# Performance work log

Measured on AMD Instinct MI355X. Metric: run time of the kernel, lower is better.

Reference implementation:

```python
import jax, jax.numpy as jnp
import numpy as np

EPS = 1e-6
MAX_TANH_ARG = 15.0


def setup_inputs() -> dict:
    key = jax.random.key(0)
    k1, k2, k3 = jax.random.split(key, 3)
    B, H, N, D = 2, 16, 2048, 64
    return {
        "q": jax.random.normal(k1, (B, H, N, D), dtype=jnp.float32),
        "k": jax.random.normal(k2, (B, H, N, D), dtype=jnp.float32),
        "v": jax.random.normal(k3, (B, H, N, D), dtype=jnp.float32),
        "c": jnp.ones((1,), dtype=jnp.float32),
        "beta": jnp.ones((1,), dtype=jnp.float32),
    }


def _exp_map(x, sqrt_c):
    # tangent space -> Poincare ball
    norm = jnp.maximum(jnp.linalg.norm(x, axis=-1, keepdims=True), EPS)
    tanh_arg = jnp.minimum(sqrt_c * norm, MAX_TANH_ARG)
    return x * (jnp.tanh(tanh_arg) / (sqrt_c * norm))


def reference(q, k, v, c, beta):
    # q, k, v: [B, H, N, D]; c, beta: [1] positive scalars
    causal, use_exp_map = True, True
    N = q.shape[2]
    c = jnp.maximum(c.astype(jnp.float32), EPS)  # [1]
    sqrt_c = jnp.sqrt(c)
    beta = beta.astype(jnp.float32)

    if use_exp_map:
        q_hyp = _exp_map(q, sqrt_c)
        k_hyp = _exp_map(k, sqrt_c)
    else:
        q_hyp, k_hyp = q, k

    q_n2 = jnp.sum(q_hyp * q_hyp, axis=-1, keepdims=True)          # [B,H,N,1]
    k_n2 = jnp.sum(k_hyp * k_hyp, axis=-1, keepdims=True)          # [B,H,N,1]
    qk = jnp.einsum('bhnd,bhmd->bhnm', q_hyp, k_hyp)               # [B,H,N,N]

    diff_n2 = jnp.maximum(q_n2 - 2.0 * qk + jnp.swapaxes(k_n2, -2, -1), 0.0)
    denom = jnp.maximum((1.0 - c * q_n2) * (1.0 - c * jnp.swapaxes(k_n2, -2, -1)), EPS)
    arg = jnp.maximum(1.0 + 2.0 * c * diff_n2 / denom, 1.0 + EPS)
    dist = jnp.arccosh(arg) / sqrt_c                               # Poincare distance
    scores = -beta * dist                                          # [B,H,N,N]

    if causal:
        mask = jnp.triu(jnp.ones((N, N), dtype=bool), k=1)
        scores = jnp.where(mask, -jnp.inf, scores)

    attn = jax.nn.softmax(scores, axis=-1)
    out = jnp.einsum('bhnm,bhmd->bhnd', attn, v)
    return out.astype(q.dtype)
```

## Files before the change

### kernel.cpp

```cpp
#include <hip/hip_runtime.h>
#include <hip/hip_bf16.h>

typedef __bf16 bf16x8 __attribute__((ext_vector_type(8)));
typedef float  f32x4  __attribute__((ext_vector_type(4)));

#define BDIM  2
#define HDIM  16
#define NDIM  2048
#define DDIM  64
#define BH    (BDIM*HDIM)
#define EPSF  1e-6f

#define QK_BLOCKS (BH * NDIM / 16)
#define V_BLOCKS  (BH * NDIM / 64)

__device__ __forceinline__ unsigned short f2bf(float x){
    union { float f; unsigned u; } a; a.f = x;
    unsigned r = a.u + 0x7fffu + ((a.u >> 16) & 1u);
    return (unsigned short)(r >> 16);
}

__global__ __launch_bounds__(256)
void prep(const float* __restrict__ q, const float* __restrict__ k,
          const float* __restrict__ v,
          unsigned short* __restrict__ qh, unsigned short* __restrict__ kh,
          unsigned short* __restrict__ vt,
          float* __restrict__ qn2, float* __restrict__ kn2,
          const float* __restrict__ cp)
{
    __shared__ float t[64][65];
    const int tid = threadIdx.x;

    if (blockIdx.x < QK_BLOCKS){
        const int row = blockIdx.x * 16 + (tid >> 4);
        const int c0  = (tid & 15) * 4;
        const float c   = fmaxf(cp[0], EPSF);
        const float sqc = sqrtf(c);

        {
            float4 x = *(const float4*)(q + (size_t)row * DDIM + c0);
            float ss = fmaf(x.x, x.x, fmaf(x.y, x.y, fmaf(x.z, x.z, x.w * x.w)));
            #pragma unroll
            for (int off = 1; off < 16; off <<= 1) ss += __shfl_xor(ss, off);
            float sn    = fmaxf(sqrtf(ss), EPSF);
            float targ  = fminf(sqc * sn, 15.0f);
            float e     = exp2f(targ * 2.885390082f);
            float th    = (e - 1.0f) * __builtin_amdgcn_rcpf(e + 1.0f);
            float scale = th * __builtin_amdgcn_rcpf(sqc * sn);
            ushort4 o;
            o.x = f2bf(x.x * scale); o.y = f2bf(x.y * scale);
            o.z = f2bf(x.z * scale); o.w = f2bf(x.w * scale);
            *(ushort4*)(qh + (size_t)row * DDIM + c0) = o;
            if ((tid & 15) == 0) qn2[row] = ss * scale * scale;
        }
        {
            float4 x = *(const float4*)(k + (size_t)row * DDIM + c0);
            float ss = fmaf(x.x, x.x, fmaf(x.y, x.y, fmaf(x.z, x.z, x.w * x.w)));
            #pragma unroll
            for (int off = 1; off < 16; off <<= 1) ss += __shfl_xor(ss, off);
            float sn    = fmaxf(sqrtf(ss), EPSF);
            float targ  = fminf(sqc * sn, 15.0f);
            float e     = exp2f(targ * 2.885390082f);
            float th    = (e - 1.0f) * __builtin_amdgcn_rcpf(e + 1.0f);
            float scale = th * __builtin_amdgcn_rcpf(sqc * sn);
            ushort4 o;
            o.x = f2bf(x.x * scale); o.y = f2bf(x.y * scale);
            o.z = f2bf(x.z * scale); o.w = f2bf(x.w * scale);
            *(ushort4*)(kh + (size_t)row * DDIM + c0) = o;
            if ((tid & 15) == 0) kn2[row] = ss * scale * scale;
        }
    } else {
        const int b  = blockIdx.x - QK_BLOCKS;
        const int bh = b >> 5;
        const int n0 = (b & 31) * 64;

        #pragma unroll
        for (int i = 0; i < 4; ++i){
            int ch  = tid + i * 256;
            int row = ch >> 4;
            int c4  = ch & 15;
            const float4 g = *(const float4*)(v + ((size_t)bh * NDIM + n0 + row) * DDIM + c4 * 4);
            t[row][c4*4 + 0] = g.x; t[row][c4*4 + 1] = g.y;
            t[row][c4*4 + 2] = g.z; t[row][c4*4 + 3] = g.w;
        }
        __syncthreads();
        #pragma unroll
        for (int i = 0; i < 4; ++i){
            int ch = tid + i * 256;
            int d  = ch >> 4;
            int nc = ch & 15;
            ushort4 o;
            o.x = f2bf(t[nc*4 + 0][d]); o.y = f2bf(t[nc*4 + 1][d]);
            o.z = f2bf(t[nc*4 + 2][d]); o.w = f2bf(t[nc*4 + 3][d]);
            *(ushort4*)(vt + ((size_t)bh * DDIM + d) * NDIM + n0 + nc * 4) = o;
        }
    }
}

__global__ __launch_bounds__(64, 4)
void hyp_attn(const unsigned short* __restrict__ qh, const unsigned short* __restrict__ kh,
              const unsigned short* __restrict__ vtg,
              const float* __restrict__ qn2g, const float* __restrict__ kn2g,
              const float* __restrict__ cp, const float* __restrict__ bp,
              float* __restrict__ out)
{
    __shared__ unsigned short pw[16 * 72];

    const int bh  = blockIdx.x;
    const int j   = 127 - (int)blockIdx.y;
    const int l   = threadIdx.x & 63;
    const int l15 = l & 15;
    const int lg  = l >> 4;

    const float c   = fmaxf(cp[0], EPSF);
    const float sqc = sqrtf(c);
    const float nb2 = -bp[0] / sqc;
    const float tc  = 2.0f * c;

    const unsigned short* khb  = kh  + (size_t)bh * (NDIM * DDIM);
    const unsigned short* vtb  = vtg + (size_t)bh * (NDIM * DDIM);
    const float*          kn2b = kn2g + (size_t)bh * NDIM;

    const int q0 = j * 16;
    const size_t qbase = ((size_t)bh * NDIM + (q0 + l15)) * DDIM;
    const bf16x8 qa0 = *(const bf16x8*)(qh + qbase + lg * 8);
    const bf16x8 qa1 = *(const bf16x8*)(qh + qbase + 32 + lg * 8);

    const int qr0 = q0 + lg * 4;
    float qn2r[4], omq[4];
    #pragma unroll
    for (int r = 0; r < 4; ++r){
        qn2r[r] = qn2g[(size_t)bh * NDIM + qr0 + r];
        omq[r]  = 1.0f - c * qn2r[r];
    }

    float m2[4], lr[4];
    f32x4 O[4];
    #pragma unroll
    for (int r = 0; r < 4; ++r){ m2[r] = -1e30f; lr[r] = 0.0f; }
    #pragma unroll
    for (int vd = 0; vd < 4; ++vd) O[vd] = (f32x4){0.f, 0.f, 0.f, 0.f};

    const int ktend = j >> 2;

    for (int kt = 0; kt <= ktend; ++kt){
        const int k0 = kt * 64;

        bf16x8 kf0[4], kf1[4];
        float  kn2m[4];
        #pragma unroll
        for (int f = 0; f < 4; ++f){
            const unsigned short* kp = khb + (size_t)(k0 + f * 16 + l15) * DDIM + lg * 8;
            kf0[f]  = *(const bf16x8*)(kp);
            kf1[f]  = *(const bf16x8*)(kp + 32);
            kn2m[f] = kn2b[k0 + f * 16 + l15];
        }

        f32x4 S[4];
        #pragma unroll
        for (int f = 0; f < 4; ++f){
            f32x4 acc = (f32x4){0.f, 0.f, 0.f, 0.f};
            acc = __builtin_amdgcn_mfma_f32_16x16x32_bf16(qa0, kf0[f], acc, 0, 0, 0);
            acc = __builtin_amdgcn_mfma_f32_16x16x32_bf16(qa1, kf1[f], acc, 0, 0, 0);
            S[f] = acc;
        }

        bf16x8 vf[2][4];
        #pragma unroll
        for (int mc = 0; mc < 2; ++mc)
            #pragma unroll
            for (int vd = 0; vd < 4; ++vd)
                vf[mc][vd] = *(const bf16x8*)(vtb + (size_t)(vd * 16 + l15) * NDIM
                                              + k0 + mc * 32 + lg * 8);

        #pragma unroll
        for (int f = 0; f < 4; ++f){
            const float kn2v = kn2m[f];
            const float omk  = 1.0f - c * kn2v;
            #pragma unroll
            for (int r = 0; r < 4; ++r){
                float diff = fmaf(-2.0f, S[f][r], qn2r[r] + kn2v);
                float den  = fmaxf(omq[r] * omk, EPSF);
                float arg  = fmaxf(fmaf(tc * diff, __builtin_amdgcn_rcpf(den), 1.0f), 1.0f + EPSF);
                float w    = arg + sqrtf(fmaf(arg, arg, -1.0f));
                S[f][r]    = nb2 * __log2f(w);
            }
        }
        if (kt == ktend){
            #pragma unroll
            for (int f = 0; f < 4; ++f){
                const int m = k0 + f * 16 + l15;
                #pragma unroll
                for (int r = 0; r < 4; ++r)
                    if (m > qr0 + r) S[f][r] = -1e30f;
            }
        }

        float rmax[4];
        #pragma unroll
        for (int r = 0; r < 4; ++r){
            rmax[r] = fmaxf(fmaxf(S[0][r], S[1][r]), fmaxf(S[2][r], S[3][r]));
            #pragma unroll
            for (int off = 1; off < 16; off <<= 1)
                rmax[r] = fmaxf(rmax[r], __shfl_xor(rmax[r], off));
        }
        bool up = (rmax[0] > m2[0]) | (rmax[1] > m2[1]) |
                  (rmax[2] > m2[2]) | (rmax[3] > m2[3]);
        if (__any(up)){
            #pragma unroll
            for (int r = 0; r < 4; ++r){
                float nm  = fmaxf(m2[r], rmax[r]);
                float scl = exp2f(m2[r] - nm);
                lr[r] *= scl; m2[r] = nm;
                #pragma unroll
                for (int vd = 0; vd < 4; ++vd) O[vd][r] *= scl;
            }
        }

        float psum[4] = {0.f, 0.f, 0.f, 0.f};
        #pragma unroll
        for (int f = 0; f < 4; ++f){
            const int fx = ((f ^ lg) << 4) + l15;
            #pragma unroll
            for (int r = 0; r < 4; ++r){
                float p = exp2f(S[f][r] - m2[r]);
                psum[r] += p;
                pw[(lg * 4 + r) * 72 + fx] = f2bf(p);
            }
        }
        #pragma unroll
        for (int r = 0; r < 4; ++r){
            #pragma unroll
            for (int off = 1; off < 16; off <<= 1)
                psum[r] += __shfl_xor(psum[r], off);
            lr[r] += psum[r];
        }

        asm volatile("s_waitcnt lgkmcnt(0)" ::: "memory");

        #pragma unroll
        for (int mc = 0; mc < 2; ++mc){
            const int f  = 2 * mc + (lg >> 1);
            const int fx = f ^ ((l15 >> 2) & 3);
            bf16x8 pa = *(const bf16x8*)&pw[l15 * 72 + fx * 16 + (lg & 1) * 8];
            #pragma unroll
            for (int vd = 0; vd < 4; ++vd)
                O[vd] = __builtin_amdgcn_mfma_f32_16x16x32_bf16(pa, vf[mc][vd], O[vd], 0, 0, 0);
        }
    }

    #pragma unroll
    for (int r = 0; r < 4; ++r){
        float rl = __builtin_amdgcn_rcpf(lr[r]);
        #pragma unroll
        for (int vd = 0; vd < 4; ++vd)
            out[((size_t)bh * NDIM + qr0 + r) * DDIM + vd * 16 + l15] = O[vd][r] * rl;
    }
}

extern "C" void kernel_launch(void* const* d_in, const int* in_sizes, int n_in,
                              void* d_out, int out_size, void* d_ws, size_t ws_size,
                              hipStream_t stream)
{
    const float* q   = (const float*)d_in[0];
    const float* k   = (const float*)d_in[1];
    const float* v   = (const float*)d_in[2];
    const float* cp  = (const float*)d_in[3];
    const float* bp  = (const float*)d_in[4];
    float*       out = (float*)d_out;

    char* ws = (char*)d_ws;
    const size_t elems = (size_t)BH * NDIM * DDIM;
    unsigned short* qh  = (unsigned short*)ws;  ws += elems * 2;
    unsigned short* kh  = (unsigned short*)ws;  ws += elems * 2;
    unsigned short* vt  = (unsigned short*)ws;  ws += elems * 2;
    float*          qn2 = (float*)ws;           ws += (size_t)BH * NDIM * 4;
    float*          kn2 = (float*)ws;

    prep<<<QK_BLOCKS + V_BLOCKS, 256, 0, stream>>>(q, k, v, qh, kh, vt, qn2, kn2, cp);
    hyp_attn<<<dim3(BH, 128), 64, 0, stream>>>(qh, kh, vt, qn2, kn2, cp, bp, out);
}
```

Measured before the change: 236.8 us.

## Compute softmax row sums via MFMA and pack two waves per block

Row sums of the softmax probabilities are now accumulated with an extra MFMA against a vector of bf16 ones. This replaces the per-row shuffle reductions and scalar adds. Blocks now hold two waves, each owning a 16-row query tile with its own LDS buffer, and the query-tile mapping is rebalanced. The row sum now uses bf16-rounded probabilities, which slightly changes numerics, and each inner iteration issues one more MFMA.

```diff
diff --git a/kernel.cpp b/kernel.cpp
--- a/kernel.cpp
+++ b/kernel.cpp
@@ -97,17 +97,20 @@
     }
 }
 
-__global__ __launch_bounds__(64, 4)
+__global__ __launch_bounds__(128, 8)
 void hyp_attn(const unsigned short* __restrict__ qh, const unsigned short* __restrict__ kh,
               const unsigned short* __restrict__ vtg,
               const float* __restrict__ qn2g, const float* __restrict__ kn2g,
               const float* __restrict__ cp, const float* __restrict__ bp,
               float* __restrict__ out)
 {
-    __shared__ unsigned short pw[16 * 72];
+    __shared__ unsigned short pw_s[2][16 * 72];
 
     const int bh  = blockIdx.x;
-    const int j   = 127 - (int)blockIdx.y;
+    const int g   = blockIdx.y;
+    const int wid = threadIdx.x >> 6;
+    const int t   = 31 - (g >> 1);
+    const int j   = 4 * t + 2 * (g & 1) + wid;
     const int l   = threadIdx.x & 63;
     const int l15 = l & 15;
     const int lg  = l >> 4;
@@ -121,6 +124,10 @@
     const unsigned short* vtb  = vtg + (size_t)bh * (NDIM * DDIM);
     const float*          kn2b = kn2g + (size_t)bh * NDIM;
 
+    bf16x8 vones;
+    #pragma unroll
+    for (int i = 0; i < 8; ++i) vones[i] = (__bf16)1.0f;
+
     const int q0 = j * 16;
     const size_t qbase = ((size_t)bh * NDIM + (q0 + l15)) * DDIM;
     const bf16x8 qa0 = *(const bf16x8*)(qh + qbase + lg * 8);
@@ -134,14 +141,16 @@
         omq[r]  = 1.0f - c * qn2r[r];
     }
 
-    float m2[4], lr[4];
-    f32x4 O[4];
-    #pragma unroll
-    for (int r = 0; r < 4; ++r){ m2[r] = -1e30f; lr[r] = 0.0f; }
+    float m2[4];
+    f32x4 O[4], Ls;
+    #pragma unroll
+    for (int r = 0; r < 4; ++r) m2[r] = -1e30f;
+    Ls = (f32x4){0.f, 0.f, 0.f, 0.f};
     #pragma unroll
     for (int vd = 0; vd < 4; ++vd) O[vd] = (f32x4){0.f, 0.f, 0.f, 0.f};
 
-    const int ktend = j >> 2;
+    unsigned short* pw = pw_s[wid];
+    const int ktend = t;
 
     for (int kt = 0; kt <= ktend; ++kt){
         const int k0 = kt * 64;
@@ -211,29 +220,21 @@
             for (int r = 0; r < 4; ++r){
                 float nm  = fmaxf(m2[r], rmax[r]);
                 float scl = exp2f(m2[r] - nm);
-                lr[r] *= scl; m2[r] = nm;
+                m2[r] = nm;
+                Ls[r] *= scl;
                 #pragma unroll
                 for (int vd = 0; vd < 4; ++vd) O[vd][r] *= scl;
             }
         }
 
-        float psum[4] = {0.f, 0.f, 0.f, 0.f};
         #pragma unroll
         for (int f = 0; f < 4; ++f){
             const int fx = ((f ^ lg) << 4) + l15;
             #pragma unroll
             for (int r = 0; r < 4; ++r){
                 float p = exp2f(S[f][r] - m2[r]);
-                psum[r] += p;
                 pw[(lg * 4 + r) * 72 + fx] = f2bf(p);
             }
-        }
-        #pragma unroll
-        for (int r = 0; r < 4; ++r){
-            #pragma unroll
-            for (int off = 1; off < 16; off <<= 1)
-                psum[r] += __shfl_xor(psum[r], off);
-            lr[r] += psum[r];
         }
 
         asm volatile("s_waitcnt lgkmcnt(0)" ::: "memory");
@@ -243,6 +244,7 @@
             const int f  = 2 * mc + (lg >> 1);
             const int fx = f ^ ((l15 >> 2) & 3);
             bf16x8 pa = *(const bf16x8*)&pw[l15 * 72 + fx * 16 + (lg & 1) * 8];
+            Ls = __builtin_amdgcn_mfma_f32_16x16x32_bf16(pa, vones, Ls, 0, 0, 0);
             #pragma unroll
             for (int vd = 0; vd < 4; ++vd)
                 O[vd] = __builtin_amdgcn_mfma_f32_16x16x32_bf16(pa, vf[mc][vd], O[vd], 0, 0, 0);
@@ -251,7 +253,7 @@
 
     #pragma unroll
     for (int r = 0; r < 4; ++r){
-        float rl = __builtin_amdgcn_rcpf(lr[r]);
+        float rl = __builtin_amdgcn_rcpf(Ls[r]);
         #pragma unroll
         for (int vd = 0; vd < 4; ++vd)
             out[((size_t)bh * NDIM + qr0 + r) * DDIM + vd * 16 + l15] = O[vd][r] * rl;
@@ -278,5 +280,5 @@
     float*          kn2 = (float*)ws;
 
     prep<<<QK_BLOCKS + V_BLOCKS, 256, 0, stream>>>(q, k, v, qh, kh, vt, qn2, kn2, cp);
-    hyp_attn<<<dim3(BH, 128), 64, 0, stream>>>(qh, kh, vt, qn2, kn2, cp, bp, out);
-}
+    hyp_attn<<<dim3(BH, 64), 128, 0, stream>>>(qh, kh, vt, qn2, kn2, cp, bp, out);
+}
```

New measurement: 380.0 us. 1.6x slower.
